# Performance work log

Hardware: AMD Instinct MI355X
Metric: run time of the kernel (lower is better)

The kernel has to match this reference:

```python
import jax, jax.numpy as jnp
import numpy as np

B, S, EMBED = 8, 2048, 512
FFN = 2048
N_QUBITS = 10
DEPTH = 2


def _apply_1q(state, mats, wire):
    # state: (N,) + (2,)*n complex; mats: (N,2,2) per-token or (2,2) shared
    s = jnp.moveaxis(state, 1 + wire, 1)
    shp = s.shape
    s = s.reshape(shp[0], 2, -1)
    if mats.ndim == 3:
        s = jnp.einsum('nab,nbr->nar', mats, s)
    else:
        s = jnp.einsum('ab,nbr->nar', mats, s)
    return jnp.moveaxis(s.reshape(shp), 1, 1 + wire)


def _cnot(state, ctrl, tgt):
    # CNOT: flip target axis on the control=1 slice
    ca, ta = 1 + ctrl, 1 + tgt
    s0 = jax.lax.index_in_dim(state, 0, axis=ca, keepdims=True)
    s1 = jax.lax.index_in_dim(state, 1, axis=ca, keepdims=True)
    s1 = jnp.flip(s1, axis=ta)
    return jnp.concatenate([s0, s1], axis=ca)


def _qlayer(x_flat, theta, n_qubits=N_QUBITS, depth=DEPTH):
    # x_flat: (N, n_qubits) RX encoding angles; theta: (n_qubits,) RY params
    N = x_flat.shape[0]
    state = jnp.zeros((N,) + (2,) * n_qubits, jnp.complex64)
    state = state.at[(slice(None),) + (0,) * n_qubits].set(1.0)
    # encoder: RX(x_i) on wire i, per-token angles
    for w in range(n_qubits):
        a = x_flat[:, w] * 0.5
        c = jnp.cos(a).astype(jnp.complex64)
        s = (-1j * jnp.sin(a)).astype(jnp.complex64)
        mats = jnp.stack([jnp.stack([c, s], -1), jnp.stack([s, c], -1)], -2)  # (N,2,2)
        state = _apply_1q(state, mats, w)
    # trainable RY(theta_w) on each wire (shared across tokens)
    for w in range(n_qubits):
        a = theta[w] * 0.5
        c, s = jnp.cos(a), jnp.sin(a)
        mat = jnp.stack([jnp.stack([c, -s]), jnp.stack([s, c])]).astype(jnp.complex64)
        state = _apply_1q(state, mat, w)
    # depth rounds of ring CNOT chain
    for _ in range(depth):
        for w in range(n_qubits - 1):
            state = _cnot(state, w, w + 1)
        state = _cnot(state, n_qubits - 1, 0)
    # MeasureAll PauliZ: <Z_w> per wire
    probs = jnp.abs(state.reshape(N, -1)) ** 2  # (N, 2^n)
    bits = (jnp.arange(2 ** n_qubits)[None, :] >> (n_qubits - 1 - jnp.arange(n_qubits))[:, None]) & 1
    z = (1 - 2 * bits).astype(probs.dtype)  # (n, 2^n)
    return probs @ z.T  # (N, n)


def setup_inputs() -> dict:
    key = jax.random.key(0)
    k = jax.random.split(key, 6)
    x = jax.random.normal(k[0], (B, S, EMBED), jnp.float32)
    ry_theta = jax.random.uniform(k[1], (N_QUBITS,), jnp.float32, 0.0, 2.0 * np.pi)
    W1 = jax.random.normal(k[2], (FFN, N_QUBITS), jnp.float32) / np.sqrt(N_QUBITS)
    b1 = jax.random.normal(k[3], (FFN,), jnp.float32) * 0.01
    W2 = jax.random.normal(k[4], (EMBED, FFN), jnp.float32) / np.sqrt(FFN)
    b2 = jax.random.normal(k[5], (EMBED,), jnp.float32) * 0.01
    return {"x": x, "ry_theta": ry_theta, "W1": W1, "b1": b1, "W2": W2, "b2": b2}


def reference(x, ry_theta, W1, b1, W2, b2):
    b, s, _ = x.shape
    xf = x.reshape(b * s, -1)[:, :N_QUBITS]  # encoder only uses first n_qubits feats
    q = _qlayer(xf, ry_theta).reshape(b, s, N_QUBITS)
    # dropout is identity at eval; linear1 -> relu -> linear2
    h = jax.nn.relu(q @ W1.T + b1)
    return h @ W2.T + b2
```

## Files before the change

### kernel.cpp

```cpp
#include <hip/hip_runtime.h>
#include <hip/hip_bf16.h>


typedef __attribute__((ext_vector_type(8))) short bf16x8;
typedef __attribute__((ext_vector_type(16))) float f32x16;
typedef __attribute__((ext_vector_type(8))) unsigned short us8;
typedef unsigned int u32;

#define NTOK  16384
#define EMBED 512
#define FFN   2048
#define NQ    10
#define BM    128
#define BN    128
#define NPAIR 16

__device__ __forceinline__ unsigned short f2bf(float f) {
  union { float f; unsigned int u; } a; a.f = f;
  unsigned int r = a.u + 0x7FFFu + ((a.u >> 16) & 1u);
  return (unsigned short)(r >> 16);
}

__device__ __forceinline__ void gload_lds16(const void* g, void* l) {
  __builtin_amdgcn_global_load_lds(
      (const __attribute__((address_space(1))) unsigned int*)g,
      (__attribute__((address_space(3))) unsigned int*)l, 16, 0, 0);
}

__global__ __launch_bounds__(256) void k_prep(const float* __restrict__ x,
                                              const float* __restrict__ theta,
                                              const float* __restrict__ W1,
                                              const float* __restrict__ b1,
                                              const float* __restrict__ W2,
                                              unsigned short* __restrict__ W2f,
                                              unsigned short* __restrict__ W1f,
                                              unsigned short* __restrict__ Qf) {
  int bb = blockIdx.x;
  if (bb < 512) {
    int gid = bb * 256 + threadIdx.x;
    int l = gid & 63, kb = (gid >> 6) & 127, tile = gid >> 13;
    int col = tile * 32 + (l & 31);
    int k0 = kb * 16 + (l >> 5) * 8;
    const float* src = W2 + (size_t)col * FFN + k0;
    float4 v0 = *(const float4*)src;
    float4 v1 = *(const float4*)(src + 4);
    us8 o;
    o[0] = f2bf(v0.x); o[1] = f2bf(v0.y); o[2] = f2bf(v0.z); o[3] = f2bf(v0.w);
    o[4] = f2bf(v1.x); o[5] = f2bf(v1.y); o[6] = f2bf(v1.z); o[7] = f2bf(v1.w);
    *(us8*)(W2f + (size_t)gid * 8) = o;
  } else if (bb < 640) {
    int gid = (bb - 512) * 256 + threadIdx.x;
    int l = gid & 63, tile = gid >> 6;
    int tok = tile * 32 + (l & 31), g = l >> 5;
    const int masks[NQ] = {0x2AB,0x3FD,0x3FA,0x3F5,0x3EA,0x3D5,0x3AA,0x355,0x2AA,0x155};
    float z[NQ], qv[NQ];
#pragma unroll
    for (int w = 0; w < NQ; ++w)
      z[w] = __builtin_cosf(x[(size_t)tok * EMBED + w]) * __builtin_cosf(theta[w]);
#pragma unroll
    for (int w = 0; w < NQ; ++w) {
      float p = 1.f;
#pragma unroll
      for (int v = 0; v < NQ; ++v)
        if ((masks[w] >> v) & 1) p *= z[v];
      qv[w] = p;
    }
    us8 o = (us8)0;
    if (g == 0) {
#pragma unroll
      for (int e = 0; e < 8; ++e) o[e] = f2bf(qv[e]);
    } else {
      o[0] = f2bf(qv[8]); o[1] = f2bf(qv[9]); o[2] = f2bf(1.f);
    }
    *(us8*)(Qf + (size_t)gid * 8) = o;
  } else {
    int gid = (bb - 640) * 256 + threadIdx.x;
    int l = gid & 63, blk = gid >> 6;
    int k = blk * 32 + (l & 31);
    int wg = (l >> 5) * 8;
    us8 o;
#pragma unroll
    for (int e = 0; e < 8; ++e) {
      int wire = wg + e;
      float v = (wire < NQ) ? W1[k * NQ + wire] : (wire == NQ ? b1[k] : 0.f);
      o[e] = f2bf(v);
    }
    *(us8*)(W1f + (size_t)gid * 8) = o;
  }
}

__global__ __launch_bounds__(512, 4) void k_fused(const unsigned short* __restrict__ Qf,
                                                  const unsigned short* __restrict__ W1f,
                                                  const unsigned short* __restrict__ W2f,
                                                  const float* __restrict__ b2,
                                                  float* __restrict__ out) {
  __shared__ short Bw[2][32 * 64 * 8];

  int bid = blockIdx.x;
  int swz = (bid & 7) * 64 + (bid >> 3);
  const int m0 = (swz >> 2) * BM;
  const int n0 = (swz & 3) * BN;
  const int tid  = threadIdx.x;
  const int lane = tid & 63;
  const int wave = tid >> 6;
  const int wm = wave >> 1, wn = wave & 1;
  const int h = lane >> 5, t31 = lane & 31;
  const int nt0 = n0 >> 5;

  bf16x8 qf = *(const bf16x8*)&Qf[(((size_t)(m0 >> 5) + wm) * 64 + lane) * 8];

  f32x16 acc[2] = {};

#define STAGE(P, B)                                                             \
  { _Pragma("unroll")                                                           \
    for (int hf = 0; hf < 4; ++hf) {                                            \
      int ch = hf * 512 + tid;                                                  \
      int tile2 = ch >> 9, kbl = (ch >> 6) & 7, ln = ch & 63;                   \
      gload_lds16(&W2f[(((size_t)(nt0 + tile2) * 128 + (P) * 8 + kbl) * 64 + ln) * 8], \
                  &Bw[B][ch * 8]);                                              \
    } }

#define HGEN1(WF, AQ0, AQ1)                                                     \
  { f32x16 zz = {};                                                             \
    f32x16 d = __builtin_amdgcn_mfma_f32_32x32x16_bf16((WF), qf, zz, 0, 0, 0);  \
    d = __builtin_elementwise_max(d, zz);                                       \
    u32 dw0, dw1, dw2, dw3, dw4, dw5, dw6, dw7;                                 \
    asm("v_cvt_pk_bf16_f32 %0, %1, %2":"=v"(dw0):"v"(d[0]),"v"(d[1]));          \
    asm("v_cvt_pk_bf16_f32 %0, %1, %2":"=v"(dw1):"v"(d[2]),"v"(d[3]));          \
    asm("v_cvt_pk_bf16_f32 %0, %1, %2":"=v"(dw2):"v"(d[4]),"v"(d[5]));          \
    asm("v_cvt_pk_bf16_f32 %0, %1, %2":"=v"(dw3):"v"(d[6]),"v"(d[7]));          \
    asm("v_cvt_pk_bf16_f32 %0, %1, %2":"=v"(dw4):"v"(d[8]),"v"(d[9]));          \
    asm("v_cvt_pk_bf16_f32 %0, %1, %2":"=v"(dw5):"v"(d[10]),"v"(d[11]));        \
    asm("v_cvt_pk_bf16_f32 %0, %1, %2":"=v"(dw6):"v"(d[12]),"v"(d[13]));        \
    asm("v_cvt_pk_bf16_f32 %0, %1, %2":"=v"(dw7):"v"(d[14]),"v"(d[15]));        \
    asm("v_permlane32_swap_b32 %0, %1" : "+v"(dw0), "+v"(dw2));                 \
    asm("v_permlane32_swap_b32 %0, %1" : "+v"(dw1), "+v"(dw3));                 \
    asm("v_permlane32_swap_b32 %0, %1" : "+v"(dw4), "+v"(dw6));                 \
    asm("v_permlane32_swap_b32 %0, %1" : "+v"(dw5), "+v"(dw7));                 \
    union { u32 u[4]; bf16x8 v; } u0, u1;                                       \
    u0.u[0]=dw0; u0.u[1]=dw1; u0.u[2]=dw2; u0.u[3]=dw3;                         \
    u1.u[0]=dw4; u1.u[1]=dw5; u1.u[2]=dw6; u1.u[3]=dw7;                         \
    AQ0 = u0.v; AQ1 = u1.v; }

#define KTBODY(Q, B, WFA, WFB)                                                  \
  { bf16x8 aq00, aq01, aq10, aq11;                                              \
    HGEN1(WFA, aq00, aq01);                                                     \
    HGEN1(WFB, aq10, aq11);                                                     \
    _Pragma("unroll")                                                           \
    for (int j = 0; j < 2; ++j) {                                               \
      bf16x8 bg0 = *(const bf16x8*)&Bw[B][(((wn * 2 + j) * 8 + (Q) * 4 + 0) * 64 + lane) * 8]; \
      bf16x8 bg1 = *(const bf16x8*)&Bw[B][(((wn * 2 + j) * 8 + (Q) * 4 + 1) * 64 + lane) * 8]; \
      bf16x8 bg2 = *(const bf16x8*)&Bw[B][(((wn * 2 + j) * 8 + (Q) * 4 + 2) * 64 + lane) * 8]; \
      bf16x8 bg3 = *(const bf16x8*)&Bw[B][(((wn * 2 + j) * 8 + (Q) * 4 + 3) * 64 + lane) * 8]; \
      __builtin_amdgcn_s_setprio(1);                                            \
      acc[j] = __builtin_amdgcn_mfma_f32_32x32x16_bf16(aq00, bg0, acc[j], 0, 0, 0); \
      acc[j] = __builtin_amdgcn_mfma_f32_32x32x16_bf16(aq01, bg1, acc[j], 0, 0, 0); \
      acc[j] = __builtin_amdgcn_mfma_f32_32x32x16_bf16(aq10, bg2, acc[j], 0, 0, 0); \
      acc[j] = __builtin_amdgcn_mfma_f32_32x32x16_bf16(aq11, bg3, acc[j], 0, 0, 0); \
      __builtin_amdgcn_s_setprio(0);                                            \
    } }

#define PAIR(P, B)                                                              \
  {                                                                             \
    asm volatile("s_waitcnt vmcnt(0)" ::: "memory");       \
    __builtin_amdgcn_s_barrier();                       \
    asm volatile("" ::: "memory");                                              \
    bf16x8 wf0 = *(const bf16x8*)&W1f[(((size_t)(P) * 4 + 0) * 64 + lane) * 8]; \
    bf16x8 wf1 = *(const bf16x8*)&W1f[(((size_t)(P) * 4 + 1) * 64 + lane) * 8]; \
    bf16x8 wf2 = *(const bf16x8*)&W1f[(((size_t)(P) * 4 + 2) * 64 + lane) * 8]; \
    bf16x8 wf3 = *(const bf16x8*)&W1f[(((size_t)(P) * 4 + 3) * 64 + lane) * 8]; \
    if ((P) + 1 < NPAIR) STAGE((P) + 1, (B) ^ 1);                               \
    KTBODY(0, B, wf0, wf1);                                                     \
    KTBODY(1, B, wf2, wf3);                                                     \
  }

  STAGE(0, 0);

  for (int p2 = 0; p2 < NPAIR / 2; ++p2) {
    PAIR(2 * p2,     0);
    PAIR(2 * p2 + 1, 1);
  }

#pragma unroll
  for (int j = 0; j < 2; ++j) {
    const int col = n0 + wn * 64 + j * 32 + t31;
    const float bbv = b2[col];
#pragma unroll
    for (int r = 0; r < 16; ++r) {
      int tok = m0 + wm * 32 + (r & 3) + 8 * (r >> 2) + 4 * h;
      out[(size_t)tok * EMBED + col] = acc[j][r] + bbv;
    }
  }
#undef STAGE
#undef HGEN1
#undef KTBODY
#undef PAIR
}

extern "C" void kernel_launch(void* const* d_in, const int* in_sizes, int n_in,
                              void* d_out, int out_size, void* d_ws, size_t ws_size,
                              hipStream_t stream) {
  const float* x     = (const float*)d_in[0];
  const float* theta = (const float*)d_in[1];
  const float* W1    = (const float*)d_in[2];
  const float* b1    = (const float*)d_in[3];
  const float* W2    = (const float*)d_in[4];
  const float* b2    = (const float*)d_in[5];
  float* out = (float*)d_out;

  char* ws = (char*)d_ws;
  unsigned short* W2f = (unsigned short*)ws;
  unsigned short* W1f = (unsigned short*)(ws + (2u << 20));
  unsigned short* Qfg = (unsigned short*)(ws + (2u << 20) + (64u << 10));

  k_prep <<<656, 256, 0, stream>>>(x, theta, W1, b1, W2, W2f, W1f, Qfg);
  k_fused<<<(NTOK / BM) * (EMBED / BN), 512, 0, stream>>>(Qfg, W1f, W2f, b2, out);
}
```

Measured before the change: 59.36 us.

## Software-pipeline hidden-activation generation one k-tile ahead of the second GEMM

Restructures the fused FFN loop so the first-layer MFMA, ReLU and bf16 pack for the next k-tile are computed while the second-layer MFMAs for the current k-tile run. W1 fragments are prefetched one k-tile ahead into double-buffered registers. The aim is to hide the dependent MFMA-to-convert latency and the W1 load latency behind independent GEMM work. The cost is higher register pressure from the extra live A-fragments and accumulators, plus more complex unrolled control flow.

```diff
diff --git a/kernel.cpp b/kernel.cpp
--- a/kernel.cpp
+++ b/kernel.cpp
@@ -110,6 +110,9 @@
   bf16x8 qf = *(const bf16x8*)&Qf[(((size_t)(m0 >> 5) + wm) * 64 + lane) * 8];
 
   f32x16 acc[2] = {};
+  bf16x8 wfX0, wfX1, wfY0, wfY1;
+  bf16x8 aqA00, aqA01, aqA10, aqA11;
+  bf16x8 aqB00, aqB01, aqB10, aqB11;
 
 #define STAGE(P, B)                                                             \
   { _Pragma("unroll")                                                           \
@@ -120,19 +123,26 @@
                   &Bw[B][ch * 8]);                                              \
     } }
 
-#define HGEN1(WF, AQ0, AQ1)                                                     \
+#define WLOAD2(R0, R1, KT)                                                      \
+  { R0 = *(const bf16x8*)&W1f[(((size_t)(KT) * 2 + 0) * 64 + lane) * 8];        \
+    R1 = *(const bf16x8*)&W1f[(((size_t)(KT) * 2 + 1) * 64 + lane) * 8]; }
+
+#define HGEN_MFMA(D, WF)                                                        \
   { f32x16 zz = {};                                                             \
-    f32x16 d = __builtin_amdgcn_mfma_f32_32x32x16_bf16((WF), qf, zz, 0, 0, 0);  \
-    d = __builtin_elementwise_max(d, zz);                                       \
+    D = __builtin_amdgcn_mfma_f32_32x32x16_bf16((WF), qf, zz, 0, 0, 0); }
+
+#define HGEN_POST(D, AQ0, AQ1)                                                  \
+  { f32x16 zz2 = {};                                                            \
+    D = __builtin_elementwise_max(D, zz2);                                      \
     u32 dw0, dw1, dw2, dw3, dw4, dw5, dw6, dw7;                                 \
-    asm("v_cvt_pk_bf16_f32 %0, %1, %2":"=v"(dw0):"v"(d[0]),"v"(d[1]));          \
-    asm("v_cvt_pk_bf16_f32 %0, %1, %2":"=v"(dw1):"v"(d[2]),"v"(d[3]));          \
-    asm("v_cvt_pk_bf16_f32 %0, %1, %2":"=v"(dw2):"v"(d[4]),"v"(d[5]));          \
-    asm("v_cvt_pk_bf16_f32 %0, %1, %2":"=v"(dw3):"v"(d[6]),"v"(d[7]));          \
-    asm("v_cvt_pk_bf16_f32 %0, %1, %2":"=v"(dw4):"v"(d[8]),"v"(d[9]));          \
-    asm("v_cvt_pk_bf16_f32 %0, %1, %2":"=v"(dw5):"v"(d[10]),"v"(d[11]));        \
-    asm("v_cvt_pk_bf16_f32 %0, %1, %2":"=v"(dw6):"v"(d[12]),"v"(d[13]));        \
-    asm("v_cvt_pk_bf16_f32 %0, %1, %2":"=v"(dw7):"v"(d[14]),"v"(d[15]));        \
+    asm("v_cvt_pk_bf16_f32 %0, %1, %2":"=v"(dw0):"v"(D[0]),"v"(D[1]));          \
+    asm("v_cvt_pk_bf16_f32 %0, %1, %2":"=v"(dw1):"v"(D[2]),"v"(D[3]));          \
+    asm("v_cvt_pk_bf16_f32 %0, %1, %2":"=v"(dw2):"v"(D[4]),"v"(D[5]));          \
+    asm("v_cvt_pk_bf16_f32 %0, %1, %2":"=v"(dw3):"v"(D[6]),"v"(D[7]));          \
+    asm("v_cvt_pk_bf16_f32 %0, %1, %2":"=v"(dw4):"v"(D[8]),"v"(D[9]));          \
+    asm("v_cvt_pk_bf16_f32 %0, %1, %2":"=v"(dw5):"v"(D[10]),"v"(D[11]));        \
+    asm("v_cvt_pk_bf16_f32 %0, %1, %2":"=v"(dw6):"v"(D[12]),"v"(D[13]));        \
+    asm("v_cvt_pk_bf16_f32 %0, %1, %2":"=v"(dw7):"v"(D[14]),"v"(D[15]));        \
     asm("v_permlane32_swap_b32 %0, %1" : "+v"(dw0), "+v"(dw2));                 \
     asm("v_permlane32_swap_b32 %0, %1" : "+v"(dw1), "+v"(dw3));                 \
     asm("v_permlane32_swap_b32 %0, %1" : "+v"(dw4), "+v"(dw6));                 \
@@ -142,44 +152,67 @@
     u1.u[0]=dw4; u1.u[1]=dw5; u1.u[2]=dw6; u1.u[3]=dw7;                         \
     AQ0 = u0.v; AQ1 = u1.v; }
 
-#define KTBODY(Q, B, WFA, WFB)                                                  \
-  { bf16x8 aq00, aq01, aq10, aq11;                                              \
-    HGEN1(WFA, aq00, aq01);                                                     \
-    HGEN1(WFB, aq10, aq11);                                                     \
-    _Pragma("unroll")                                                           \
-    for (int j = 0; j < 2; ++j) {                                               \
-      bf16x8 bg0 = *(const bf16x8*)&Bw[B][(((wn * 2 + j) * 8 + (Q) * 4 + 0) * 64 + lane) * 8]; \
-      bf16x8 bg1 = *(const bf16x8*)&Bw[B][(((wn * 2 + j) * 8 + (Q) * 4 + 1) * 64 + lane) * 8]; \
-      bf16x8 bg2 = *(const bf16x8*)&Bw[B][(((wn * 2 + j) * 8 + (Q) * 4 + 2) * 64 + lane) * 8]; \
-      bf16x8 bg3 = *(const bf16x8*)&Bw[B][(((wn * 2 + j) * 8 + (Q) * 4 + 3) * 64 + lane) * 8]; \
-      __builtin_amdgcn_s_setprio(1);                                            \
-      acc[j] = __builtin_amdgcn_mfma_f32_32x32x16_bf16(aq00, bg0, acc[j], 0, 0, 0); \
-      acc[j] = __builtin_amdgcn_mfma_f32_32x32x16_bf16(aq01, bg1, acc[j], 0, 0, 0); \
-      acc[j] = __builtin_amdgcn_mfma_f32_32x32x16_bf16(aq10, bg2, acc[j], 0, 0, 0); \
-      acc[j] = __builtin_amdgcn_mfma_f32_32x32x16_bf16(aq11, bg3, acc[j], 0, 0, 0); \
-      __builtin_amdgcn_s_setprio(0);                                            \
-    } }
-
-#define PAIR(P, B)                                                              \
-  {                                                                             \
-    asm volatile("s_waitcnt vmcnt(0)" ::: "memory");       \
+#define GEMMJ(J, Q, B, A00, A01, A10, A11)                                      \
+  { bf16x8 bg0 = *(const bf16x8*)&Bw[B][(((wn * 2 + (J)) * 8 + (Q) * 4 + 0) * 64 + lane) * 8]; \
+    bf16x8 bg1 = *(const bf16x8*)&Bw[B][(((wn * 2 + (J)) * 8 + (Q) * 4 + 1) * 64 + lane) * 8]; \
+    bf16x8 bg2 = *(const bf16x8*)&Bw[B][(((wn * 2 + (J)) * 8 + (Q) * 4 + 2) * 64 + lane) * 8]; \
+    bf16x8 bg3 = *(const bf16x8*)&Bw[B][(((wn * 2 + (J)) * 8 + (Q) * 4 + 3) * 64 + lane) * 8]; \
+    __builtin_amdgcn_s_setprio(1);                                              \
+    acc[J] = __builtin_amdgcn_mfma_f32_32x32x16_bf16(A00, bg0, acc[J], 0, 0, 0); \
+    acc[J] = __builtin_amdgcn_mfma_f32_32x32x16_bf16(A01, bg1, acc[J], 0, 0, 0); \
+    acc[J] = __builtin_amdgcn_mfma_f32_32x32x16_bf16(A10, bg2, acc[J], 0, 0, 0); \
+    acc[J] = __builtin_amdgcn_mfma_f32_32x32x16_bf16(A11, bg3, acc[J], 0, 0, 0); \
+    __builtin_amdgcn_s_setprio(0); }
+
+#define KT_EVEN(P, B, MORE)                                                     \
+  { if (MORE) WLOAD2(wfY0, wfY1, 2 * (P) + 2);                                  \
+    f32x16 d0;                                                                  \
+    HGEN_MFMA(d0, wfX0);                                                        \
+    GEMMJ(0, 0, B, aqA00, aqA01, aqA10, aqA11);                                 \
+    HGEN_POST(d0, aqB00, aqB01);                                                \
+    f32x16 d1;                                                                  \
+    HGEN_MFMA(d1, wfX1);                                                        \
+    GEMMJ(1, 0, B, aqA00, aqA01, aqA10, aqA11);                                 \
+    HGEN_POST(d1, aqB10, aqB11); }
+
+#define KT_ODD(P, B, MORE)                                                      \
+  { if (MORE) WLOAD2(wfX0, wfX1, 2 * (P) + 3);                                  \
+    f32x16 d0;                                                                  \
+    if (MORE) { HGEN_MFMA(d0, wfY0); }                                          \
+    GEMMJ(0, 1, B, aqB00, aqB01, aqB10, aqB11);                                 \
+    if (MORE) { HGEN_POST(d0, aqA00, aqA01); }                                  \
+    f32x16 d1;                                                                  \
+    if (MORE) { HGEN_MFMA(d1, wfY1); }                                          \
+    GEMMJ(1, 1, B, aqB00, aqB01, aqB10, aqB11);                                 \
+    if (MORE) { HGEN_POST(d1, aqA10, aqA11); } }
+
+#define PAIR(P, B, MORE)                                                        \
+  { asm volatile("s_waitcnt vmcnt(0)" ::: "memory");       \
     __builtin_amdgcn_s_barrier();                       \
     asm volatile("" ::: "memory");                                              \
-    bf16x8 wf0 = *(const bf16x8*)&W1f[(((size_t)(P) * 4 + 0) * 64 + lane) * 8]; \
-    bf16x8 wf1 = *(const bf16x8*)&W1f[(((size_t)(P) * 4 + 1) * 64 + lane) * 8]; \
-    bf16x8 wf2 = *(const bf16x8*)&W1f[(((size_t)(P) * 4 + 2) * 64 + lane) * 8]; \
-    bf16x8 wf3 = *(const bf16x8*)&W1f[(((size_t)(P) * 4 + 3) * 64 + lane) * 8]; \
-    if ((P) + 1 < NPAIR) STAGE((P) + 1, (B) ^ 1);                               \
-    KTBODY(0, B, wf0, wf1);                                                     \
-    KTBODY(1, B, wf2, wf3);                                                     \
-  }
-
-  STAGE(0, 0);
-
-  for (int p2 = 0; p2 < NPAIR / 2; ++p2) {
-    PAIR(2 * p2,     0);
-    PAIR(2 * p2 + 1, 1);
-  }
+    if (MORE) STAGE((P) + 1, (B) ^ 1);                                          \
+    KT_EVEN(P, B, MORE);                                                        \
+    KT_ODD(P, B, MORE); }
+
+  {
+    bf16x8 wfP0, wfP1;
+    WLOAD2(wfP0, wfP1, 0);
+    WLOAD2(wfX0, wfX1, 1);
+    STAGE(0, 0);
+    f32x16 d0;
+    HGEN_MFMA(d0, wfP0);
+    HGEN_POST(d0, aqA00, aqA01);
+    f32x16 d1;
+    HGEN_MFMA(d1, wfP1);
+    HGEN_POST(d1, aqA10, aqA11);
+  }
+
+  for (int p2 = 0; p2 < 7; ++p2) {
+    PAIR(2 * p2,     0, 1);
+    PAIR(2 * p2 + 1, 1, 1);
+  }
+  PAIR(14, 0, 1);
+  PAIR(15, 1, 0);
 
 #pragma unroll
   for (int j = 0; j < 2; ++j) {
@@ -192,8 +225,12 @@
     }
   }
 #undef STAGE
-#undef HGEN1
-#undef KTBODY
+#undef WLOAD2
+#undef HGEN_MFMA
+#undef HGEN_POST
+#undef GEMMJ
+#undef KT_EVEN
+#undef KT_ODD
 #undef PAIR
 }
 
```

Result: slower. 138.3 us (+133.0%).
